# Kernel optimization log

Measured on AMD Instinct MI355X. Metric: run time of the kernel, lower is better.

## Reference

```python
import jax, jax.numpy as jnp
import numpy as np

N, E, T, B = 10000, 80000, 240000, 32
HF, EMB = 256, 64
EDGE_BINS, ANG_BINS = 80, 40
N_CONV = 12  # 4 alignn layers x 2 EGGC + 4 gcn EGGC


def layernorm(x, scale, bias):
    m = x.mean(-1, keepdims=True)
    v = ((x - m) ** 2).mean(-1, keepdims=True)
    return (x - m) / jnp.sqrt(v + 1e-5) * scale + bias


def mlp_layer(x, W, b, ln):
    # Linear -> LayerNorm -> SiLU
    return jax.nn.silu(layernorm(x @ W + b, ln[0], ln[1]))


def rbf(x, vmin, vmax, bins):
    centers = jnp.linspace(vmin, vmax, bins)
    gamma = 0.5 / ((vmax - vmin) / bins) ** 2
    return jnp.exp(-gamma * (x[..., None] - centers) ** 2)


def eggc(W, b, ln_s, ln_b, src, dst, h, e, n_nodes):
    """Edge-gated graph conv. W:[5,F,F] b:[5,F] order: src_gate,dst_gate,edge_gate,src_update,dst_update.
    ln_s/ln_b:[2,F] order: edges, nodes."""
    e_src = h @ W[0] + b[0]
    e_dst = h @ W[1] + b[1]
    sigma = jax.nn.sigmoid(e_src[src] + e_dst[dst] + e @ W[2] + b[2])  # [n_edges, F]
    e_out = layernorm(sigma * e, ln_s[0], ln_b[0])
    Bh = h @ W[4] + b[4]  # dst_update
    sum_sh = jax.ops.segment_sum(Bh[src] * sigma, dst, num_segments=n_nodes)
    sum_s = jax.ops.segment_sum(sigma, dst, num_segments=n_nodes)
    h_out = h @ W[3] + b[3] + sum_sh / (sum_s + 1e-8)  # src_update + gated mean
    return layernorm(h_out, ln_s[1], ln_b[1]), e_out


def setup_inputs() -> dict:
    key = jax.random.key(0)
    ks = jax.random.split(key, 24)
    rn = lambda k, shp: (jax.random.normal(k, shp, dtype=jnp.float32) * 0.05)
    ln_init = lambda f: jnp.stack([jnp.ones((f,), jnp.float32), jnp.zeros((f,), jnp.float32)])
    inp = {
        'atom_features': jax.random.normal(ks[0], (N, 92), dtype=jnp.float32),
        'bondlength': jax.random.uniform(ks[1], (E,), dtype=jnp.float32) * 8.0,
        'angle_h': jax.random.uniform(ks[2], (T,), dtype=jnp.float32) * 2.0 - 1.0,
        'src': jax.random.randint(ks[3], (E,), 0, N, dtype=jnp.int32),
        'dst': jax.random.randint(ks[4], (E,), 0, N, dtype=jnp.int32),
        'lg_src': jax.random.randint(ks[5], (T,), 0, E, dtype=jnp.int32),
        'lg_dst': jax.random.randint(ks[6], (T,), 0, E, dtype=jnp.int32),
        'graph_ids': jnp.sort(jax.random.randint(ks[7], (N,), 0, B)).astype(jnp.int32),
        'atom_W': rn(ks[8], (92, HF)), 'atom_b': jnp.zeros((HF,), jnp.float32), 'atom_ln': ln_init(HF),
        'edge_W1': rn(ks[9], (EDGE_BINS, EMB)), 'edge_b1': jnp.zeros((EMB,), jnp.float32), 'edge_ln1': ln_init(EMB),
        'edge_W2': rn(ks[10], (EMB, HF)), 'edge_b2': jnp.zeros((HF,), jnp.float32), 'edge_ln2': ln_init(HF),
        'ang_W1': rn(ks[11], (ANG_BINS, EMB)), 'ang_b1': jnp.zeros((EMB,), jnp.float32), 'ang_ln1': ln_init(EMB),
        'ang_W2': rn(ks[12], (EMB, HF)), 'ang_b2': jnp.zeros((HF,), jnp.float32), 'ang_ln2': ln_init(HF),
        'conv_W': rn(ks[13], (N_CONV, 5, HF, HF)),
        'conv_b': jnp.zeros((N_CONV, 5, HF), jnp.float32),
        'conv_ln_s': jnp.ones((N_CONV, 2, HF), jnp.float32),
        'conv_ln_b': jnp.zeros((N_CONV, 2, HF), jnp.float32),
    }
    return inp


def reference(atom_features, bondlength, angle_h, src, dst, lg_src, lg_dst, graph_ids,
              atom_W, atom_b, atom_ln, edge_W1, edge_b1, edge_ln1, edge_W2, edge_b2, edge_ln2,
              ang_W1, ang_b1, ang_ln1, ang_W2, ang_b2, ang_ln2,
              conv_W, conv_b, conv_ln_s, conv_ln_b):
    n_nodes = atom_features.shape[0]
    n_edges = bondlength.shape[0]
    # embeddings
    z = mlp_layer(mlp_layer(rbf(angle_h, -1.0, 1.0, ANG_BINS), ang_W1, ang_b1, ang_ln1), ang_W2, ang_b2, ang_ln2)
    x = mlp_layer(atom_features, atom_W, atom_b, atom_ln)
    y = mlp_layer(mlp_layer(rbf(bondlength, 0.0, 8.0, EDGE_BINS), edge_W1, edge_b1, edge_ln1), edge_W2, edge_b2, edge_ln2)
    # 4 ALIGNN layers: edge_update on line graph, then node_update on graph
    for i in range(4):
        j = 2 * i
        y, z = eggc(conv_W[j], conv_b[j], conv_ln_s[j], conv_ln_b[j], lg_src, lg_dst, y, z, n_edges)
        j = 2 * i + 1
        x, y = eggc(conv_W[j], conv_b[j], conv_ln_s[j], conv_ln_b[j], src, dst, x, y, n_nodes)
    # 4 GCN layers
    for i in range(4):
        j = 8 + i
        x, y = eggc(conv_W[j], conv_b[j], conv_ln_s[j], conv_ln_b[j], src, dst, x, y, n_nodes)
    # AvgPooling readout per graph
    sums = jax.ops.segment_sum(x, graph_ids, num_segments=B)
    counts = jax.ops.segment_sum(jnp.ones((n_nodes,), x.dtype), graph_ids, num_segments=B)
    return sums / jnp.maximum(counts, 1.0)[:, None]
```

## Files before the change

### kernel.cpp

```cpp
#include <hip/hip_runtime.h>
#include <hip/hip_bf16.h>

typedef unsigned short u16;
typedef unsigned int u32;
typedef __attribute__((ext_vector_type(8))) short short8;
typedef __attribute__((ext_vector_type(4))) float f32x4;

__device__ __forceinline__ float bf2f(u16 u) { return __uint_as_float(((u32)u) << 16); }
__device__ __forceinline__ u16 f2bf(float f) {
  u32 x = __float_as_uint(f);
  return (u16)((x + 0x7FFFu + ((x >> 16) & 1u)) >> 16);
}
__device__ __forceinline__ void up4(uint2 r, float* o) {
  o[0] = bf2f((u16)(r.x & 0xFFFF)); o[1] = bf2f((u16)(r.x >> 16));
  o[2] = bf2f((u16)(r.y & 0xFFFF)); o[3] = bf2f((u16)(r.y >> 16));
}
__device__ __forceinline__ uint2 pk4(const float* o) {
  uint2 r;
  r.x = (u32)f2bf(o[0]) | ((u32)f2bf(o[1]) << 16);
  r.y = (u32)f2bf(o[2]) | ((u32)f2bf(o[3]) << 16);
  return r;
}
__device__ __forceinline__ float wsum64(float v) {
#pragma unroll
  for (int o = 32; o > 0; o >>= 1) v += __shfl_xor(v, o, 64);
  return v;
}
__device__ __forceinline__ float sigm(float x) { return 1.0f / (1.0f + __expf(-x)); }

__global__ __launch_bounds__(256) void fill_kernel(float* __restrict__ out, int n, float v) {
  int i = blockIdx.x * 256 + threadIdx.x;
  if (i < n) out[i] = v;
}

__global__ __launch_bounds__(256) void wtrans(const float* __restrict__ in,
                                              u16* __restrict__ out, int R, int Ccols) {
  __shared__ float t[64][65];
  const float* ip = in + (size_t)blockIdx.z * R * Ccols;
  u16* op = out + (size_t)blockIdx.z * R * Ccols;
  int kb = blockIdx.x * 64, nb = blockIdx.y * 64;
  int lr = threadIdx.x >> 4, lc = (threadIdx.x & 15) * 4;
#pragma unroll
  for (int p = 0; p < 4; ++p) {
    int k = lr + p * 16;
    float4 v = *(const float4*)(ip + (size_t)(kb + k) * Ccols + nb + lc);
    t[k][lc + 0] = v.x; t[k][lc + 1] = v.y; t[k][lc + 2] = v.z; t[k][lc + 3] = v.w;
  }
  __syncthreads();
#pragma unroll
  for (int p = 0; p < 4; ++p) {
    int n = lr + p * 16;
    uint2 pk;
    pk.x = (u32)f2bf(t[lc + 0][n]) | ((u32)f2bf(t[lc + 1][n]) << 16);
    pk.y = (u32)f2bf(t[lc + 2][n]) | ((u32)f2bf(t[lc + 3][n]) << 16);
    *(uint2*)(op + (size_t)(nb + n) * R + kb + lc) = pk;
  }
}

__global__ __launch_bounds__(256) void csr_hist(const int* __restrict__ dst,
                                                int* __restrict__ hist, int ne) {
  int e = blockIdx.x * 256 + threadIdx.x;
  if (e < ne) atomicAdd(&hist[dst[e]], 1);
}
__global__ __launch_bounds__(1024) void scan1(const int* __restrict__ in,
                                              int* __restrict__ out1, int* __restrict__ bsum, int n) {
  __shared__ int s[1024];
  int i = blockIdx.x * 1024 + threadIdx.x;
  int v = (i < n) ? in[i] : 0;
  s[threadIdx.x] = v; __syncthreads();
  for (int off = 1; off < 1024; off <<= 1) {
    int t = (threadIdx.x >= (u32)off) ? s[threadIdx.x - off] : 0;
    __syncthreads();
    s[threadIdx.x] += t;
    __syncthreads();
  }
  if (i < n) out1[i] = s[threadIdx.x];
  if (threadIdx.x == 1023) bsum[blockIdx.x] = s[1023];
}
__global__ __launch_bounds__(128) void scan2(int* __restrict__ bsum, int nb) {
  __shared__ int s[128];
  int v = (threadIdx.x < (u32)nb) ? bsum[threadIdx.x] : 0;
  s[threadIdx.x] = v; __syncthreads();
  for (int off = 1; off < 128; off <<= 1) {
    int t = (threadIdx.x >= (u32)off) ? s[threadIdx.x - off] : 0;
    __syncthreads();
    s[threadIdx.x] += t;
    __syncthreads();
  }
  if (threadIdx.x < (u32)nb) bsum[threadIdx.x] = threadIdx.x ? s[threadIdx.x - 1] : 0;
}
__global__ __launch_bounds__(256) void scan3(int* __restrict__ offs,
                                             const int* __restrict__ bsum, int n) {
  int i = blockIdx.x * 256 + threadIdx.x;
  if (i == 0) offs[0] = 0;
  if (i < n) offs[1 + i] += bsum[i >> 10];
}
__global__ __launch_bounds__(256) void csr_scatter(const int* __restrict__ dst,
                                                   int* __restrict__ cursor,
                                                   const int* __restrict__ offs,
                                                   int* __restrict__ eid, int ne) {
  int e = blockIdx.x * 256 + threadIdx.x;
  if (e < ne) {
    int d = dst[e];
    int p = offs[d] + atomicAdd(&cursor[d], 1);
    eid[p] = e;
  }
}
__global__ __launch_bounds__(256) void inv_perm(const int* __restrict__ eid,
                                                int* __restrict__ pos, int n) {
  int i = blockIdx.x * 256 + threadIdx.x;
  if (i < n) pos[eid[i]] = i;
}
__global__ __launch_bounds__(256) void remap_k(const int* __restrict__ idx,
                                               const int* __restrict__ map,
                                               int* __restrict__ out, int n) {
  int i = blockIdx.x * 256 + threadIdx.x;
  if (i < n) out[i] = map[idx[i]];
}
__global__ __launch_bounds__(256) void compose_src(const int* __restrict__ eid,
                                                   const int* __restrict__ srcv,
                                                   const int* __restrict__ map,
                                                   int* __restrict__ out, int n) {
  int i = blockIdx.x * 256 + threadIdx.x;
  if (i < n) {
    int s = srcv[eid[i]];
    out[i] = map ? map[s] : s;
  }
}

__global__ __launch_bounds__(256) void embed_s1(
    const float* __restrict__ xin, const float* __restrict__ W1,
    const float* __restrict__ b1, const float* __restrict__ ln1,
    u16* __restrict__ t1, int rows, int bins, float vmin, float vmax,
    const int* __restrict__ perm) {
  int row = (blockIdx.x * 256 + threadIdx.x) >> 6;
  if (row >= rows) return;
  int lane = threadIdx.x & 63;
  float xv = xin[row];
  float rng = vmax - vmin;
  float step = rng / (float)(bins - 1);
  float gamma = 0.5f * ((float)bins / rng) * ((float)bins / rng);
  float rb = 0.f, rb2 = 0.f;
  if (lane < bins) {
    float d = xv - (vmin + lane * step);
    rb = __expf(-gamma * d * d);
  }
  if (bins > 64 && lane < bins - 64) {
    float d = xv - (vmin + (lane + 64) * step);
    rb2 = __expf(-gamma * d * d);
  }
  float u = b1[lane];
  int k1 = bins < 64 ? bins : 64;
  for (int k = 0; k < k1; ++k) {
    float rv = __shfl(rb, k, 64);
    u = fmaf(rv, W1[k * 64 + lane], u);
  }
  for (int k = 64; k < bins; ++k) {
    float rv = __shfl(rb2, k - 64, 64);
    u = fmaf(rv, W1[k * 64 + lane], u);
  }
  float s = wsum64(u), s2 = wsum64(u * u);
  float m = s * (1.f / 64.f), var = s2 * (1.f / 64.f) - m * m;
  float t = (u - m) * rsqrtf(var + 1e-5f) * ln1[lane] + ln1[64 + lane];
  int orow = perm ? perm[row] : row;
  t1[(size_t)orow * 64 + lane] = f2bf(t * sigm(t));
}

__global__ __launch_bounds__(256) void ln_silu(u16* __restrict__ buf,
                                               const float* __restrict__ ln, int rows) {
  int row = (blockIdx.x * 256 + threadIdx.x) >> 6;
  if (row >= rows) return;
  int lane = threadIdx.x & 63;
  int f = lane * 4;
  float v[4];
  up4(*(const uint2*)(buf + (size_t)row * 256 + f), v);
  float s = wsum64(v[0] + v[1] + v[2] + v[3]);
  float s2 = wsum64(v[0] * v[0] + v[1] * v[1] + v[2] * v[2] + v[3] * v[3]);
  float m = s * (1.f / 256.f);
  float rs = rsqrtf(s2 * (1.f / 256.f) - m * m + 1e-5f);
  float o[4];
#pragma unroll
  for (int k = 0; k < 4; ++k) {
    float t = (v[k] - m) * rs * ln[f + k] + ln[256 + f + k];
    o[k] = t * sigm(t);
  }
  *(uint2*)(buf + (size_t)row * 256 + f) = pk4(o);
}

__global__ __launch_bounds__(256) void atom_embed_kernel(
    const float* __restrict__ af, const float* __restrict__ W,
    const float* __restrict__ b, const float* __restrict__ ln,
    u16* __restrict__ out, int rows) {
  int row = blockIdx.x;
  if (row >= rows) return;
  __shared__ float a_s[92];
  __shared__ float red[8];
  int tid = threadIdx.x;
  if (tid < 92) a_s[tid] = af[(size_t)row * 92 + tid];
  __syncthreads();
  float v = b[tid];
#pragma unroll 4
  for (int k = 0; k < 92; ++k) v = fmaf(a_s[k], W[k * 256 + tid], v);
  float s = wsum64(v), s2 = wsum64(v * v);
  int lane = tid & 63, wid = tid >> 6;
  if (lane == 0) { red[wid] = s; red[4 + wid] = s2; }
  __syncthreads();
  s = red[0] + red[1] + red[2] + red[3];
  s2 = red[4] + red[5] + red[6] + red[7];
  float m = s * (1.f / 256.f), var = s2 * (1.f / 256.f) - m * m;
  float t = (v - m) * rsqrtf(var + 1e-5f) * ln[tid] + ln[256 + tid];
  out[(size_t)row * 256 + tid] = f2bf(t * sigm(t));
}

__global__ __launch_bounds__(256) void mfma_gemm(
    const u16* __restrict__ A, const u16* __restrict__ Wt,
    const float* __restrict__ bias, u16* __restrict__ C,
    int M, int K, int ldc, int slab_step) {
  int bm = blockIdx.x * 128;
  if (bm >= M) return;
  int bn = blockIdx.y * 128;
  int slab = (bn >> 8) * slab_step;
  const u16* Wp = Wt + (size_t)slab * 256 * K + (size_t)(bn & 255) * K;
  const float* bp = bias + slab * 256 + (bn & 255);
  int tid = threadIdx.x;
  int w = tid >> 6, lane = tid & 63;
  int q = lane >> 4, r = lane & 15;
  int m0 = (w & 1) * 64;
  int n0 = (w >> 1) * 64;
  const u16* aptr[4];
#pragma unroll
  for (int mi = 0; mi < 4; ++mi) {
    int m = bm + m0 + mi * 16 + r;
    m = m < M - 1 ? m : M - 1;
    aptr[mi] = A + (size_t)m * K + q * 8;
  }
  const u16* wptr[4];
#pragma unroll
  for (int ni = 0; ni < 4; ++ni)
    wptr[ni] = Wp + (size_t)(n0 + ni * 16 + r) * K + q * 8;
  f32x4 acc[4][4] = {};
  for (int kb = 0; kb < K; kb += 32) {
    short8 bfr[4], afr[4];
#pragma unroll
    for (int mi = 0; mi < 4; ++mi) bfr[mi] = *(const short8*)(aptr[mi] + kb);
#pragma unroll
    for (int ni = 0; ni < 4; ++ni) afr[ni] = *(const short8*)(wptr[ni] + kb);
#pragma unroll
    for (int mi = 0; mi < 4; ++mi)
#pragma unroll
      for (int ni = 0; ni < 4; ++ni)
        acc[mi][ni] = __builtin_amdgcn_mfma_f32_16x16x32_bf16(afr[ni], bfr[mi],
                                                              acc[mi][ni], 0, 0, 0);
  }
#pragma unroll
  for (int mi = 0; mi < 4; ++mi) {
    int m = bm + m0 + mi * 16 + r;
    if (m < M) {
#pragma unroll
      for (int ni = 0; ni < 4; ++ni) {
        int n = n0 + ni * 16 + q * 4;
        float4 bv = *(const float4*)(bp + n);
        uint2 o;
        o.x = (u32)f2bf(acc[mi][ni].x + bv.x) | ((u32)f2bf(acc[mi][ni].y + bv.y) << 16);
        o.y = (u32)f2bf(acc[mi][ni].z + bv.z) | ((u32)f2bf(acc[mi][ni].w + bv.w) << 16);
        *(uint2*)(C + (size_t)m * ldc + bn + n) = o;
      }
    }
  }
}

__global__ __launch_bounds__(512) void mega_eggc(
    u16* __restrict__ h, u16* __restrict__ e,
    const u16* __restrict__ G0Bh,
    const u16* __restrict__ Wt13, const float* __restrict__ b13,
    const u16* __restrict__ Wt2, const float* __restrict__ b2v,
    const int* __restrict__ src_perm, const int* __restrict__ offs,
    const float* __restrict__ lnS, const float* __restrict__ lnB, int nn) {
  __shared__ u16 g1ah[16][520];
  __shared__ u16 pe[64][264];
  int tid = threadIdx.x;
  int w = tid >> 6, lane = tid & 63;
  int q = lane >> 4, r = lane & 15;
  int v0 = blockIdx.x * 16;

  {
    int mrow = v0 + r; if (mrow > nn - 1) mrow = nn - 1;
    const u16* arow = h + (size_t)mrow * 256 + q * 8;
    f32x4 acc[4] = {};
    for (int kb = 0; kb < 256; kb += 32) {
      short8 af = *(const short8*)(arow + kb);
#pragma unroll
      for (int t = 0; t < 4; ++t) {
        int ng = (4 * w + t) * 16 + r;
        const u16* wrow = Wt13 + (size_t)(ng >> 8) * 2 * 65536 +
                          (size_t)(ng & 255) * 256 + q * 8;
        short8 wf = *(const short8*)(wrow + kb);
        acc[t] = __builtin_amdgcn_mfma_f32_16x16x32_bf16(wf, af, acc[t], 0, 0, 0);
      }
    }
#pragma unroll
    for (int t = 0; t < 4; ++t) {
      int nb = (4 * w + t) * 16 + q * 4;
      const float* bp = b13 + (nb >> 8) * 2 * 256 + (nb & 255);
      float o[4] = {acc[t].x + bp[0], acc[t].y + bp[1], acc[t].z + bp[2], acc[t].w + bp[3]};
      *(uint2*)&g1ah[r][nb] = pk4(o);
    }
  }
  __syncthreads();

  int f = lane * 4;
  int r0 = offs[v0];
  int vend = v0 + 16 < nn ? v0 + 16 : nn;
  int r1 = offs[vend];
  int vA = v0 + w * 2, vB = vA + 1;
  int eA0 = vA < nn ? offs[vA] : 0, eA1 = vA < nn ? offs[vA + 1] : 0;
  int eB0 = vB < nn ? offs[vB] : 0, eB1 = vB < nn ? offs[vB + 1] : 0;
  float sshA[4] = {0, 0, 0, 0}, ssmA[4] = {0, 0, 0, 0};
  float sshB[4] = {0, 0, 0, 0}, ssmB[4] = {0, 0, 0, 0};
  float lwe[4], lbe[4];
#pragma unroll
  for (int k = 0; k < 4; ++k) { lwe[k] = lnS[f + k]; lbe[k] = lnB[f + k]; }

  for (int ec = r0; ec < r1; ec += 64) {
    {
      const u16* w0p = Wt2 + (size_t)((2 * w) * 16 + r) * 256 + q * 8;
      const u16* w1p = Wt2 + (size_t)((2 * w + 1) * 16 + r) * 256 + q * 8;
      f32x4 acc[4][2] = {};
      for (int kb = 0; kb < 256; kb += 32) {
        short8 wf0 = *(const short8*)(w0p + kb);
        short8 wf1 = *(const short8*)(w1p + kb);
#pragma unroll
        for (int mt = 0; mt < 4; ++mt) {
          int erow = ec + mt * 16 + r;
          if (erow > r1 - 1) erow = r1 - 1;
          short8 af = *(const short8*)(e + (size_t)erow * 256 + kb + q * 8);
          acc[mt][0] = __builtin_amdgcn_mfma_f32_16x16x32_bf16(wf0, af, acc[mt][0], 0, 0, 0);
          acc[mt][1] = __builtin_amdgcn_mfma_f32_16x16x32_bf16(wf1, af, acc[mt][1], 0, 0, 0);
        }
      }
#pragma unroll
      for (int mt = 0; mt < 4; ++mt)
#pragma unroll
        for (int nt = 0; nt < 2; ++nt) {
          int nb = (2 * w + nt) * 16 + q * 4;
          float o[4] = {acc[mt][nt].x + b2v[nb], acc[mt][nt].y + b2v[nb + 1],
                        acc[mt][nt].z + b2v[nb + 2], acc[mt][nt].w + b2v[nb + 3]};
          *(uint2*)&pe[mt * 16 + r][nb] = pk4(o);
        }
    }
    __syncthreads();
    int ce = ec + 64 < r1 ? ec + 64 : r1;
#pragma unroll
    for (int jj = 0; jj < 2; ++jj) {
      int vv = jj ? vB : vA;
      int i0 = jj ? eB0 : eA0, i1 = jj ? eB1 : eA1;
      int lo = i0 > ec ? i0 : ec, hi = i1 < ce ? i1 : ce;
      for (int i = lo; i < hi; ++i) {
        int sv = src_perm[i];
        float g0[4], bh[4], pv[4], ev[4], g1v[4];
        up4(*(const uint2*)(G0Bh + (size_t)sv * 512 + f), g0);
        up4(*(const uint2*)(G0Bh + (size_t)sv * 512 + 256 + f), bh);
        up4(*(const uint2*)&pe[i - ec][f], pv);
        up4(*(const uint2*)(e + (size_t)i * 256 + f), ev);
        up4(*(const uint2*)&g1ah[vv - v0][f], g1v);
        float t[4];
        float ssum = 0.f, s2sum = 0.f;
#pragma unroll
        for (int k = 0; k < 4; ++k) {
          float sg = sigm(g0[k] + g1v[k] + pv[k]);
          t[k] = sg * ev[k];
          if (jj) { sshB[k] = fmaf(bh[k], sg, sshB[k]); ssmB[k] += sg; }
          else    { sshA[k] = fmaf(bh[k], sg, sshA[k]); ssmA[k] += sg; }
          ssum += t[k]; s2sum += t[k] * t[k];
        }
        float s1 = wsum64(ssum), s2 = wsum64(s2sum);
        float mn = s1 * (1.f / 256.f);
        float rs = rsqrtf(s2 * (1.f / 256.f) - mn * mn + 1e-5f);
        float o[4];
#pragma unroll
        for (int k = 0; k < 4; ++k) o[k] = (t[k] - mn) * rs * lwe[k] + lbe[k];
        *(uint2*)(e + (size_t)i * 256 + f) = pk4(o);
      }
    }
    __syncthreads();
  }
#pragma unroll
  for (int jj = 0; jj < 2; ++jj) {
    int vv = jj ? vB : vA;
    if (vv < nn) {
      float ah[4], tt[4];
      up4(*(const uint2*)&g1ah[vv - v0][256 + f], ah);
      float ssum = 0.f, s2sum = 0.f;
#pragma unroll
      for (int k = 0; k < 4; ++k) {
        float sh = jj ? sshB[k] : sshA[k];
        float sm = jj ? ssmB[k] : ssmA[k];
        tt[k] = ah[k] + sh / (sm + 1e-8f);
        ssum += tt[k]; s2sum += tt[k] * tt[k];
      }
      float s1 = wsum64(ssum), s2 = wsum64(s2sum);
      float mn = s1 * (1.f / 256.f);
      float rs = rsqrtf(s2 * (1.f / 256.f) - mn * mn + 1e-5f);
      float o[4];
#pragma unroll
      for (int k = 0; k < 4; ++k)
        o[k] = (tt[k] - mn) * rs * lnS[256 + f + k] + lnB[256 + f + k];
      *(uint2*)(h + (size_t)vv * 256 + f) = pk4(o);
    }
  }
}

__global__ __launch_bounds__(256) void pool_acc(
    const u16* __restrict__ x, const int* __restrict__ gid,
    float* __restrict__ out, float* __restrict__ cnt, int n) {
  int v = (blockIdx.x * 256 + threadIdx.x) >> 6;
  if (v >= n) return;
  int lane = threadIdx.x & 63;
  int f = lane * 4;
  int g = gid[v];
  float xv[4];
  up4(*(const uint2*)(x + (size_t)v * 256 + f), xv);
  float* p = out + (size_t)g * 256 + f;
  unsafeAtomicAdd(p + 0, xv[0]);
  unsafeAtomicAdd(p + 1, xv[1]);
  unsafeAtomicAdd(p + 2, xv[2]);
  unsafeAtomicAdd(p + 3, xv[3]);
  if (lane == 0) unsafeAtomicAdd(cnt + g, 1.0f);
}
__global__ __launch_bounds__(256) void pool_div(float* __restrict__ out,
                                                const float* __restrict__ cnt, int n) {
  int i = blockIdx.x * blockDim.x + threadIdx.x;
  if (i < n) out[i] /= fmaxf(cnt[i >> 8], 1.0f);
}

extern "C" void kernel_launch(void* const* d_in, const int* in_sizes, int n_in,
                              void* d_out, int out_size, void* d_ws, size_t ws_size,
                              hipStream_t stream) {
  const float* atom_features = (const float*)d_in[0];
  const float* bondlength    = (const float*)d_in[1];
  const float* angle_h       = (const float*)d_in[2];
  const int*   src           = (const int*)d_in[3];
  const int*   dst           = (const int*)d_in[4];
  const int*   lg_src        = (const int*)d_in[5];
  const int*   lg_dst        = (const int*)d_in[6];
  const int*   gid           = (const int*)d_in[7];
  const float* atom_W  = (const float*)d_in[8];
  const float* atom_b  = (const float*)d_in[9];
  const float* atom_ln = (const float*)d_in[10];
  const float* edge_W1 = (const float*)d_in[11];
  const float* edge_b1 = (const float*)d_in[12];
  const float* edge_ln1= (const float*)d_in[13];
  const float* edge_W2 = (const float*)d_in[14];
  const float* edge_b2 = (const float*)d_in[15];
  const float* edge_ln2= (const float*)d_in[16];
  const float* ang_W1  = (const float*)d_in[17];
  const float* ang_b1  = (const float*)d_in[18];
  const float* ang_ln1 = (const float*)d_in[19];
  const float* ang_W2  = (const float*)d_in[20];
  const float* ang_b2  = (const float*)d_in[21];
  const float* ang_ln2 = (const float*)d_in[22];
  const float* conv_W  = (const float*)d_in[23];
  const float* conv_b  = (const float*)d_in[24];
  const float* conv_lns= (const float*)d_in[25];
  const float* conv_lnb= (const float*)d_in[26];

  int N = in_sizes[0] / 92;
  int E = in_sizes[1];
  int T = in_sizes[2];

  char* ws = (char*)d_ws;
  size_t o = 0;
  auto alloc = [&](size_t bytes) { size_t r = o; o = (o + bytes + 255) & ~(size_t)255; return r; };
  u16* z     = (u16*)(ws + alloc((size_t)T * 512));
  u16* y     = (u16*)(ws + alloc((size_t)E * 512));
  u16* x     = (u16*)(ws + alloc((size_t)N * 512));
  int* offsL = (int*)(ws + alloc((size_t)(E + 1) * 4));
  int* offsA = (int*)(ws + alloc((size_t)(N + 1) * 4));
  int* spL   = (int*)(ws + alloc((size_t)T * 4));
  int* spA   = (int*)(ws + alloc((size_t)E * 4));
  int* pA    = (int*)(ws + alloc((size_t)E * 4));
  int* pL    = (int*)(ws + alloc((size_t)T * 4));
  int* eidL  = (int*)(ws + alloc((size_t)T * 4));
  int* eidA  = (int*)(ws + alloc((size_t)E * 4));
  int* ldSt  = (int*)(ws + alloc((size_t)T * 4));
  int* tmp   = (int*)(ws + alloc((size_t)(E > N ? E : N) * 4));
  int* bsum  = (int*)(ws + alloc(1024));
  float* cnt = (float*)(ws + alloc(1024));
  u16* WtAll = (u16*)(ws + alloc((size_t)12 * 5 * 65536 * 2));
  u16* WtAng = (u16*)(ws + alloc((size_t)16384 * 2));
  u16* WtEdg = (u16*)(ws + alloc((size_t)16384 * 2));
  size_t scratch_base = o;
  size_t need = scratch_base + (size_t)E * 1024;
  {
    size_t embed_need = scratch_base + ((size_t)T + E) * 128;
    if (embed_need > need) need = embed_need;
  }
  if (ws_size < need) {
    fill_kernel<<<(out_size + 255) / 256, 256, 0, stream>>>(
        (float*)d_out, out_size, (float)(ws_size >> 20));
    return;
  }

  wtrans<<<dim3(4, 4, 60), 256, 0, stream>>>(conv_W, WtAll, 256, 256);
  wtrans<<<dim3(1, 4, 1), 256, 0, stream>>>(ang_W2, WtAng, 64, 256);
  wtrans<<<dim3(1, 4, 1), 256, 0, stream>>>(edge_W2, WtEdg, 64, 256);

  auto build_csr = [&](const int* dvec, int ne_, int nn_, int* offs_, int* eid_) {
    hipMemsetAsync(tmp, 0, (size_t)nn_ * 4, stream);
    csr_hist<<<(ne_ + 255) / 256, 256, 0, stream>>>(dvec, tmp, ne_);
    int nb = (nn_ + 1023) / 1024;
    scan1<<<nb, 1024, 0, stream>>>(tmp, offs_ + 1, bsum, nn_);
    scan2<<<1, 128, 0, stream>>>(bsum, nb);
    scan3<<<(nn_ + 255) / 256, 256, 0, stream>>>(offs_, bsum, nn_);
    hipMemsetAsync(tmp, 0, (size_t)nn_ * 4, stream);
    csr_scatter<<<(ne_ + 255) / 256, 256, 0, stream>>>(dvec, tmp, offs_, eid_, ne_);
  };
  build_csr(dst, E, N, offsA, eidA);
  inv_perm<<<(E + 255) / 256, 256, 0, stream>>>(eidA, pA, E);
  compose_src<<<(E + 255) / 256, 256, 0, stream>>>(eidA, src, nullptr, spA, E);
  remap_k<<<(T + 255) / 256, 256, 0, stream>>>(lg_dst, pA, ldSt, T);
  build_csr(ldSt, T, E, offsL, eidL);
  inv_perm<<<(T + 255) / 256, 256, 0, stream>>>(eidL, pL, T);
  compose_src<<<(T + 255) / 256, 256, 0, stream>>>(eidL, lg_src, pA, spL, T);

  u16* t1T = (u16*)(ws + scratch_base);
  u16* t1E = t1T + (size_t)T * 64;
  embed_s1<<<(T + 3) / 4, 256, 0, stream>>>(angle_h, ang_W1, ang_b1, ang_ln1,
                                            t1T, T, 40, -1.f, 1.f, pL);
  embed_s1<<<(E + 3) / 4, 256, 0, stream>>>(bondlength, edge_W1, edge_b1, edge_ln1,
                                            t1E, E, 80, 0.f, 8.f, pA);
  mfma_gemm<<<dim3((T + 127) / 128, 2), 256, 0, stream>>>(
      t1T, WtAng, ang_b2, z, T, 64, 256, 1);
  mfma_gemm<<<dim3((E + 127) / 128, 2), 256, 0, stream>>>(
      t1E, WtEdg, edge_b2, y, E, 64, 256, 1);
  ln_silu<<<(T + 3) / 4, 256, 0, stream>>>(z, ang_ln2, T);
  ln_silu<<<(E + 3) / 4, 256, 0, stream>>>(y, edge_ln2, E);
  atom_embed_kernel<<<N, 256, 0, stream>>>(atom_features, atom_W, atom_b, atom_ln, x, N);

  u16* G0Bh = (u16*)(ws + scratch_base);
  for (int l = 0; l < 12; ++l) {
    const u16* WtL  = WtAll + (size_t)l * 5 * 65536;
    const float* bl = conv_b + (size_t)l * 5 * 256;
    const float* lnS = conv_lns + (size_t)l * 512;
    const float* lnB = conv_lnb + (size_t)l * 512;
    bool line = (l < 8) && ((l & 1) == 0);
    u16* h = line ? y : x;
    u16* e = line ? z : y;
    const int* sperm = line ? spL : spA;
    const int* offs  = line ? offsL : offsA;
    int nn = line ? E : N;

    mfma_gemm<<<dim3((nn + 127) / 128, 4), 256, 0, stream>>>(
        h, WtL, bl, G0Bh, nn, 256, 512, 4);
    mega_eggc<<<(nn + 15) / 16, 512, 0, stream>>>(
        h, e, G0Bh, WtL + 65536, bl + 256, WtL + 2 * 65536, bl + 2 * 256,
        sperm, offs, lnS, lnB, nn);
  }

  hipMemsetAsync(d_out, 0, (size_t)out_size * sizeof(float), stream);
  hipMemsetAsync(cnt, 0, 256 * sizeof(float), stream);
  pool_acc<<<(N + 3) / 4, 256, 0, stream>>>(x, gid, (float*)d_out, cnt, N);
  pool_div<<<(out_size + 255) / 256, 256, 0, stream>>>((float*)d_out, cnt, out_size);
}
```

Baseline: 5.469 ms.

## Shrink edge chunk to 32, raise occupancy, prefetch next edge gather

Cuts the per-chunk edge tile in the fused EGGC kernel from 64 to 32 rows. This halves the shared pe buffer and the MFMA accumulator registers, and adds a min-blocks launch bound hint to raise occupancy. The per-edge loop now software-prefetches the next edge's gathered G0/Bh and e rows, and hoists the per-node g1 load out of the loop, to hide gather latency. In exchange there are twice as many chunk iterations and syncthreads, and the Wt2 weight fragments are reloaded per chunk. Forcing occupancy may also cause register spills.

Result: slower. 6.757 ms (+23.6%).

```diff
diff --git a/kernel.cpp b/kernel.cpp
--- a/kernel.cpp
+++ b/kernel.cpp
@@ -269,7 +269,7 @@
   }
 }
 
-__global__ __launch_bounds__(512) void mega_eggc(
+__global__ __launch_bounds__(512, 6) void mega_eggc(
     u16* __restrict__ h, u16* __restrict__ e,
     const u16* __restrict__ G0Bh,
     const u16* __restrict__ Wt13, const float* __restrict__ b13,
@@ -277,7 +277,7 @@
     const int* __restrict__ src_perm, const int* __restrict__ offs,
     const float* __restrict__ lnS, const float* __restrict__ lnB, int nn) {
   __shared__ u16 g1ah[16][520];
-  __shared__ u16 pe[64][264];
+  __shared__ u16 pe[32][264];
   int tid = threadIdx.x;
   int w = tid >> 6, lane = tid & 63;
   int q = lane >> 4, r = lane & 15;
@@ -321,25 +321,27 @@
 #pragma unroll
   for (int k = 0; k < 4; ++k) { lwe[k] = lnS[f + k]; lbe[k] = lnB[f + k]; }
 
-  for (int ec = r0; ec < r1; ec += 64) {
+  for (int ec = r0; ec < r1; ec += 32) {
     {
       const u16* w0p = Wt2 + (size_t)((2 * w) * 16 + r) * 256 + q * 8;
       const u16* w1p = Wt2 + (size_t)((2 * w + 1) * 16 + r) * 256 + q * 8;
-      f32x4 acc[4][2] = {};
+      int er0 = ec + r;      if (er0 > r1 - 1) er0 = r1 - 1;
+      int er1 = ec + 16 + r; if (er1 > r1 - 1) er1 = r1 - 1;
+      const u16* ap0 = e + (size_t)er0 * 256 + q * 8;
+      const u16* ap1 = e + (size_t)er1 * 256 + q * 8;
+      f32x4 acc[2][2] = {};
       for (int kb = 0; kb < 256; kb += 32) {
         short8 wf0 = *(const short8*)(w0p + kb);
         short8 wf1 = *(const short8*)(w1p + kb);
-#pragma unroll
-        for (int mt = 0; mt < 4; ++mt) {
-          int erow = ec + mt * 16 + r;
-          if (erow > r1 - 1) erow = r1 - 1;
-          short8 af = *(const short8*)(e + (size_t)erow * 256 + kb + q * 8);
-          acc[mt][0] = __builtin_amdgcn_mfma_f32_16x16x32_bf16(wf0, af, acc[mt][0], 0, 0, 0);
-          acc[mt][1] = __builtin_amdgcn_mfma_f32_16x16x32_bf16(wf1, af, acc[mt][1], 0, 0, 0);
-        }
+        short8 af0 = *(const short8*)(ap0 + kb);
+        short8 af1 = *(const short8*)(ap1 + kb);
+        acc[0][0] = __builtin_amdgcn_mfma_f32_16x16x32_bf16(wf0, af0, acc[0][0], 0, 0, 0);
+        acc[0][1] = __builtin_amdgcn_mfma_f32_16x16x32_bf16(wf1, af0, acc[0][1], 0, 0, 0);
+        acc[1][0] = __builtin_amdgcn_mfma_f32_16x16x32_bf16(wf0, af1, acc[1][0], 0, 0, 0);
+        acc[1][1] = __builtin_amdgcn_mfma_f32_16x16x32_bf16(wf1, af1, acc[1][1], 0, 0, 0);
       }
 #pragma unroll
-      for (int mt = 0; mt < 4; ++mt)
+      for (int mt = 0; mt < 2; ++mt)
 #pragma unroll
         for (int nt = 0; nt < 2; ++nt) {
           int nb = (2 * w + nt) * 16 + q * 4;
@@ -349,20 +351,30 @@
         }
     }
     __syncthreads();
-    int ce = ec + 64 < r1 ? ec + 64 : r1;
+    int ce = ec + 32 < r1 ? ec + 32 : r1;
 #pragma unroll
     for (int jj = 0; jj < 2; ++jj) {
       int vv = jj ? vB : vA;
       int i0 = jj ? eB0 : eA0, i1 = jj ? eB1 : eA1;
       int lo = i0 > ec ? i0 : ec, hi = i1 < ce ? i1 : ce;
+      if (lo >= hi) continue;
+      float g1v[4];
+      up4(*(const uint2*)&g1ah[vv - v0][f], g1v);
+      int sv0 = src_perm[lo];
+      uint2 rg0 = *(const uint2*)(G0Bh + (size_t)sv0 * 512 + f);
+      uint2 rbh = *(const uint2*)(G0Bh + (size_t)sv0 * 512 + 256 + f);
+      uint2 rev = *(const uint2*)(e + (size_t)lo * 256 + f);
       for (int i = lo; i < hi; ++i) {
-        int sv = src_perm[i];
-        float g0[4], bh[4], pv[4], ev[4], g1v[4];
-        up4(*(const uint2*)(G0Bh + (size_t)sv * 512 + f), g0);
-        up4(*(const uint2*)(G0Bh + (size_t)sv * 512 + 256 + f), bh);
+        uint2 cg0 = rg0, cbh = rbh, cev = rev;
+        if (i + 1 < hi) {
+          int sv = src_perm[i + 1];
+          rg0 = *(const uint2*)(G0Bh + (size_t)sv * 512 + f);
+          rbh = *(const uint2*)(G0Bh + (size_t)sv * 512 + 256 + f);
+          rev = *(const uint2*)(e + (size_t)(i + 1) * 256 + f);
+        }
+        float g0[4], bh[4], pv[4], ev[4];
+        up4(cg0, g0); up4(cbh, bh); up4(cev, ev);
         up4(*(const uint2*)&pe[i - ec][f], pv);
-        up4(*(const uint2*)(e + (size_t)i * 256 + f), ev);
-        up4(*(const uint2*)&g1ah[vv - v0][f], g1v);
         float t[4];
         float ssum = 0.f, s2sum = 0.f;
 #pragma unroll
```

## Split EGGC into line/atom kernels with 16-lane-per-edge vectorized gather

Applied to the files above, without the earlier changes.

Reworks the edge-gating phase so each 16-lane group handles one destination node's edges with 16 features per lane. Two groups split the edges of a node and combine their partial sums with a shuffle. Gathers use 128-bit loads with one-step prefetch of the next source row, and the per-edge layernorm reduces across 16 lanes instead of 64. For the atom graph (small N), all four node projections are computed by one wider GEMM via a slab map instead of in-kernel MFMA, which removes redundant work from the mega kernel. The cost is higher register pressure and two code paths to maintain.

Measured after the change: 5.316 ms. -2.8%, faster.

```diff
diff --git a/kernel.cpp b/kernel.cpp
--- a/kernel.cpp
+++ b/kernel.cpp
@@ -21,9 +21,28 @@
   r.y = (u32)f2bf(o[2]) | ((u32)f2bf(o[3]) << 16);
   return r;
 }
+__device__ __forceinline__ void up8(uint4 r, float* o) {
+  o[0] = bf2f((u16)(r.x & 0xFFFF)); o[1] = bf2f((u16)(r.x >> 16));
+  o[2] = bf2f((u16)(r.y & 0xFFFF)); o[3] = bf2f((u16)(r.y >> 16));
+  o[4] = bf2f((u16)(r.z & 0xFFFF)); o[5] = bf2f((u16)(r.z >> 16));
+  o[6] = bf2f((u16)(r.w & 0xFFFF)); o[7] = bf2f((u16)(r.w >> 16));
+}
+__device__ __forceinline__ uint4 pk8(const float* o) {
+  uint4 r;
+  r.x = (u32)f2bf(o[0]) | ((u32)f2bf(o[1]) << 16);
+  r.y = (u32)f2bf(o[2]) | ((u32)f2bf(o[3]) << 16);
+  r.z = (u32)f2bf(o[4]) | ((u32)f2bf(o[5]) << 16);
+  r.w = (u32)f2bf(o[6]) | ((u32)f2bf(o[7]) << 16);
+  return r;
+}
 __device__ __forceinline__ float wsum64(float v) {
 #pragma unroll
   for (int o = 32; o > 0; o >>= 1) v += __shfl_xor(v, o, 64);
+  return v;
+}
+__device__ __forceinline__ float wsum16(float v) {
+#pragma unroll
+  for (int o = 8; o > 0; o >>= 1) v += __shfl_xor(v, o, 64);
   return v;
 }
 __device__ __forceinline__ float sigm(float x) { return 1.0f / (1.0f + __expf(-x)); }
@@ -215,11 +234,11 @@
 __global__ __launch_bounds__(256) void mfma_gemm(
     const u16* __restrict__ A, const u16* __restrict__ Wt,
     const float* __restrict__ bias, u16* __restrict__ C,
-    int M, int K, int ldc, int slab_step) {
+    int M, int K, int ldc, u32 smap) {
   int bm = blockIdx.x * 128;
   if (bm >= M) return;
   int bn = blockIdx.y * 128;
-  int slab = (bn >> 8) * slab_step;
+  int slab = (smap >> ((bn >> 8) * 8)) & 0xFF;
   const u16* Wp = Wt + (size_t)slab * 256 * K + (size_t)(bn & 255) * K;
   const float* bp = bias + slab * 256 + (bn & 255);
   int tid = threadIdx.x;
@@ -269,20 +288,20 @@
   }
 }
 
-__global__ __launch_bounds__(512) void mega_eggc(
-    u16* __restrict__ h, u16* __restrict__ e,
-    const u16* __restrict__ G0Bh,
+__global__ __launch_bounds__(512) void mega_line(
+    u16* __restrict__ h, u16* __restrict__ e, const u16* __restrict__ G0Bh,
     const u16* __restrict__ Wt13, const float* __restrict__ b13,
     const u16* __restrict__ Wt2, const float* __restrict__ b2v,
     const int* __restrict__ src_perm, const int* __restrict__ offs,
     const float* __restrict__ lnS, const float* __restrict__ lnB, int nn) {
   __shared__ u16 g1ah[16][520];
   __shared__ u16 pe[64][264];
+  __shared__ int oloc[17];
   int tid = threadIdx.x;
   int w = tid >> 6, lane = tid & 63;
   int q = lane >> 4, r = lane & 15;
   int v0 = blockIdx.x * 16;
-
+  if (tid < 17) { int v = v0 + tid; oloc[tid] = offs[v < nn ? v : nn]; }
   {
     int mrow = v0 + r; if (mrow > nn - 1) mrow = nn - 1;
     const u16* arow = h + (size_t)mrow * 256 + q * 8;
@@ -307,19 +326,20 @@
     }
   }
   __syncthreads();
-
-  int f = lane * 4;
-  int r0 = offs[v0];
-  int vend = v0 + 16 < nn ? v0 + 16 : nn;
-  int r1 = offs[vend];
-  int vA = v0 + w * 2, vB = vA + 1;
-  int eA0 = vA < nn ? offs[vA] : 0, eA1 = vA < nn ? offs[vA + 1] : 0;
-  int eB0 = vB < nn ? offs[vB] : 0, eB1 = vB < nn ? offs[vB + 1] : 0;
-  float sshA[4] = {0, 0, 0, 0}, ssmA[4] = {0, 0, 0, 0};
-  float sshB[4] = {0, 0, 0, 0}, ssmB[4] = {0, 0, 0, 0};
-  float lwe[4], lbe[4];
-#pragma unroll
-  for (int k = 0; k < 4; ++k) { lwe[k] = lnS[f + k]; lbe[k] = lnB[f + k]; }
+  int gl = lane & 15;
+  int qg = lane >> 4;
+  int dd = w * 2 + (qg >> 1);
+  int half = qg & 1;
+  int vv = v0 + dd;
+  int fb = gl * 16;
+  int r0 = oloc[0], r1 = oloc[16];
+  int d0 = oloc[dd], d1 = oloc[dd + 1];
+  float lwe[16], lbe[16];
+#pragma unroll
+  for (int k = 0; k < 16; ++k) { lwe[k] = lnS[fb + k]; lbe[k] = lnB[fb + k]; }
+  uint4 g1p0 = *(const uint4*)&g1ah[dd][fb];
+  uint4 g1p1 = *(const uint4*)&g1ah[dd][fb + 8];
+  float ssh[16] = {}, ssm[16] = {};
 
   for (int ec = r0; ec < r1; ec += 64) {
     {
@@ -349,64 +369,216 @@
         }
     }
     __syncthreads();
-    int ce = ec + 64 < r1 ? ec + 64 : r1;
-#pragma unroll
-    for (int jj = 0; jj < 2; ++jj) {
-      int vv = jj ? vB : vA;
-      int i0 = jj ? eB0 : eA0, i1 = jj ? eB1 : eA1;
-      int lo = i0 > ec ? i0 : ec, hi = i1 < ce ? i1 : ce;
-      for (int i = lo; i < hi; ++i) {
-        int sv = src_perm[i];
-        float g0[4], bh[4], pv[4], ev[4], g1v[4];
-        up4(*(const uint2*)(G0Bh + (size_t)sv * 512 + f), g0);
-        up4(*(const uint2*)(G0Bh + (size_t)sv * 512 + 256 + f), bh);
-        up4(*(const uint2*)&pe[i - ec][f], pv);
-        up4(*(const uint2*)(e + (size_t)i * 256 + f), ev);
-        up4(*(const uint2*)&g1ah[vv - v0][f], g1v);
-        float t[4];
-        float ssum = 0.f, s2sum = 0.f;
-#pragma unroll
-        for (int k = 0; k < 4; ++k) {
-          float sg = sigm(g0[k] + g1v[k] + pv[k]);
-          t[k] = sg * ev[k];
-          if (jj) { sshB[k] = fmaf(bh[k], sg, sshB[k]); ssmB[k] += sg; }
-          else    { sshA[k] = fmaf(bh[k], sg, sshA[k]); ssmA[k] += sg; }
-          ssum += t[k]; s2sum += t[k] * t[k];
+    {
+      int ce = ec + 64 < r1 ? ec + 64 : r1;
+      int i0 = d0 > ec ? d0 : ec;
+      int i1 = d1 < ce ? d1 : ce;
+      int is = i0 + half;
+      if (is < i1) {
+        int sv = src_perm[is];
+        uint4 pg0a = *(const uint4*)(G0Bh + (size_t)sv * 512 + fb);
+        uint4 pg0b = *(const uint4*)(G0Bh + (size_t)sv * 512 + fb + 8);
+        uint4 pbha = *(const uint4*)(G0Bh + (size_t)sv * 512 + 256 + fb);
+        uint4 pbhb = *(const uint4*)(G0Bh + (size_t)sv * 512 + 256 + fb + 8);
+        for (int i = is; i < i1; i += 2) {
+          uint4 cg0a = pg0a, cg0b = pg0b, cbha = pbha, cbhb = pbhb;
+          if (i + 2 < i1) {
+            int sv2 = src_perm[i + 2];
+            pg0a = *(const uint4*)(G0Bh + (size_t)sv2 * 512 + fb);
+            pg0b = *(const uint4*)(G0Bh + (size_t)sv2 * 512 + fb + 8);
+            pbha = *(const uint4*)(G0Bh + (size_t)sv2 * 512 + 256 + fb);
+            pbhb = *(const uint4*)(G0Bh + (size_t)sv2 * 512 + 256 + fb + 8);
+          }
+          float g0[16], bh[16], pv[16], ev[16], g1v[16];
+          up8(cg0a, g0); up8(cg0b, g0 + 8);
+          up8(cbha, bh); up8(cbhb, bh + 8);
+          up8(*(const uint4*)&pe[i - ec][fb], pv);
+          up8(*(const uint4*)&pe[i - ec][fb + 8], pv + 8);
+          up8(*(const uint4*)(e + (size_t)i * 256 + fb), ev);
+          up8(*(const uint4*)(e + (size_t)i * 256 + fb + 8), ev + 8);
+          up8(g1p0, g1v); up8(g1p1, g1v + 8);
+          float t[16];
+          float ssum = 0.f, s2sum = 0.f;
+#pragma unroll
+          for (int k = 0; k < 16; ++k) {
+            float sg = sigm(g0[k] + g1v[k] + pv[k]);
+            t[k] = sg * ev[k];
+            ssh[k] = fmaf(bh[k], sg, ssh[k]);
+            ssm[k] += sg;
+            ssum += t[k]; s2sum += t[k] * t[k];
+          }
+          float s1 = wsum16(ssum), s2 = wsum16(s2sum);
+          float mn = s1 * (1.f / 256.f);
+          float rs = rsqrtf(s2 * (1.f / 256.f) - mn * mn + 1e-5f);
+          float o[16];
+#pragma unroll
+          for (int k = 0; k < 16; ++k) o[k] = (t[k] - mn) * rs * lwe[k] + lbe[k];
+          *(uint4*)(e + (size_t)i * 256 + fb) = pk8(o);
+          *(uint4*)(e + (size_t)i * 256 + fb + 8) = pk8(o + 8);
         }
-        float s1 = wsum64(ssum), s2 = wsum64(s2sum);
-        float mn = s1 * (1.f / 256.f);
-        float rs = rsqrtf(s2 * (1.f / 256.f) - mn * mn + 1e-5f);
-        float o[4];
-#pragma unroll
-        for (int k = 0; k < 4; ++k) o[k] = (t[k] - mn) * rs * lwe[k] + lbe[k];
-        *(uint2*)(e + (size_t)i * 256 + f) = pk4(o);
       }
     }
     __syncthreads();
   }
 #pragma unroll
-  for (int jj = 0; jj < 2; ++jj) {
-    int vv = jj ? vB : vA;
-    if (vv < nn) {
-      float ah[4], tt[4];
-      up4(*(const uint2*)&g1ah[vv - v0][256 + f], ah);
-      float ssum = 0.f, s2sum = 0.f;
-#pragma unroll
-      for (int k = 0; k < 4; ++k) {
-        float sh = jj ? sshB[k] : sshA[k];
-        float sm = jj ? ssmB[k] : ssmA[k];
-        tt[k] = ah[k] + sh / (sm + 1e-8f);
-        ssum += tt[k]; s2sum += tt[k] * tt[k];
+  for (int k = 0; k < 16; ++k) {
+    ssh[k] += __shfl_xor(ssh[k], 16, 64);
+    ssm[k] += __shfl_xor(ssm[k], 16, 64);
+  }
+  if (half == 0 && vv < nn) {
+    float ah[16], tt[16];
+    up8(*(const uint4*)&g1ah[dd][256 + fb], ah);
+    up8(*(const uint4*)&g1ah[dd][256 + fb + 8], ah + 8);
+    float ssum = 0.f, s2sum = 0.f;
+#pragma unroll
+    for (int k = 0; k < 16; ++k) {
+      tt[k] = ah[k] + ssh[k] / (ssm[k] + 1e-8f);
+      ssum += tt[k]; s2sum += tt[k] * tt[k];
+    }
+    float s1 = wsum16(ssum), s2 = wsum16(s2sum);
+    float mn = s1 * (1.f / 256.f);
+    float rs = rsqrtf(s2 * (1.f / 256.f) - mn * mn + 1e-5f);
+    float o[16];
+#pragma unroll
+    for (int k = 0; k < 16; ++k)
+      o[k] = (tt[k] - mn) * rs * lnS[256 + fb + k] + lnB[256 + fb + k];
+    *(uint4*)(h + (size_t)vv * 256 + fb) = pk8(o);
+    *(uint4*)(h + (size_t)vv * 256 + fb + 8) = pk8(o + 8);
+  }
+}
+
+__global__ __launch_bounds__(512) void mega_atom(
+    u16* __restrict__ h, u16* __restrict__ e, const u16* __restrict__ GAll,
+    const u16* __restrict__ Wt2, const float* __restrict__ b2v,
+    const int* __restrict__ src_perm, const int* __restrict__ offs,
+    const float* __restrict__ lnS, const float* __restrict__ lnB, int nn) {
+  __shared__ u16 pe[64][264];
+  __shared__ int oloc[17];
+  int tid = threadIdx.x;
+  int w = tid >> 6, lane = tid & 63;
+  int q = lane >> 4, r = lane & 15;
+  int v0 = blockIdx.x * 16;
+  if (tid < 17) { int v = v0 + tid; oloc[tid] = offs[v < nn ? v : nn]; }
+  __syncthreads();
+  int gl = lane & 15;
+  int qg = lane >> 4;
+  int dd = w * 2 + (qg >> 1);
+  int half = qg & 1;
+  int vv = v0 + dd;
+  int fb = gl * 16;
+  int r0 = oloc[0], r1 = oloc[16];
+  int d0 = oloc[dd], d1 = oloc[dd + 1];
+  float lwe[16], lbe[16];
+#pragma unroll
+  for (int k = 0; k < 16; ++k) { lwe[k] = lnS[fb + k]; lbe[k] = lnB[fb + k]; }
+  int vc = vv < nn ? vv : nn - 1;
+  uint4 g1p0 = *(const uint4*)(GAll + (size_t)vc * 1024 + 256 + fb);
+  uint4 g1p1 = *(const uint4*)(GAll + (size_t)vc * 1024 + 256 + fb + 8);
+  float ssh[16] = {}, ssm[16] = {};
+
+  for (int ec = r0; ec < r1; ec += 64) {
+    {
+      const u16* w0p = Wt2 + (size_t)((2 * w) * 16 + r) * 256 + q * 8;
+      const u16* w1p = Wt2 + (size_t)((2 * w + 1) * 16 + r) * 256 + q * 8;
+      f32x4 acc[4][2] = {};
+      for (int kb = 0; kb < 256; kb += 32) {
+        short8 wf0 = *(const short8*)(w0p + kb);
+        short8 wf1 = *(const short8*)(w1p + kb);
+#pragma unroll
+        for (int mt = 0; mt < 4; ++mt) {
+          int erow = ec + mt * 16 + r;
+          if (erow > r1 - 1) erow = r1 - 1;
+          short8 af = *(const short8*)(e + (size_t)erow * 256 + kb + q * 8);
+          acc[mt][0] = __builtin_amdgcn_mfma_f32_16x16x32_bf16(wf0, af, acc[mt][0], 0, 0, 0);
+          acc[mt][1] = __builtin_amdgcn_mfma_f32_16x16x32_bf16(wf1, af, acc[mt][1], 0, 0, 0);
+        }
       }
-      float s1 = wsum64(ssum), s2 = wsum64(s2sum);
-      float mn = s1 * (1.f / 256.f);
-      float rs = rsqrtf(s2 * (1.f / 256.f) - mn * mn + 1e-5f);
-      float o[4];
-#pragma unroll
-      for (int k = 0; k < 4; ++k)
-        o[k] = (tt[k] - mn) * rs * lnS[256 + f + k] + lnB[256 + f + k];
-      *(uint2*)(h + (size_t)vv * 256 + f) = pk4(o);
-    }
+#pragma unroll
+      for (int mt = 0; mt < 4; ++mt)
+#pragma unroll
+        for (int nt = 0; nt < 2; ++nt) {
+          int nb = (2 * w + nt) * 16 + q * 4;
+          float o[4] = {acc[mt][nt].x + b2v[nb], acc[mt][nt].y + b2v[nb + 1],
+                        acc[mt][nt].z + b2v[nb + 2], acc[mt][nt].w + b2v[nb + 3]};
+          *(uint2*)&pe[mt * 16 + r][nb] = pk4(o);
+        }
+    }
+    __syncthreads();
+    {
+      int ce = ec + 64 < r1 ? ec + 64 : r1;
+      int i0 = d0 > ec ? d0 : ec;
+      int i1 = d1 < ce ? d1 : ce;
+      int is = i0 + half;
+      if (is < i1) {
+        int sv = src_perm[is];
+        uint4 pg0a = *(const uint4*)(GAll + (size_t)sv * 1024 + fb);
+        uint4 pg0b = *(const uint4*)(GAll + (size_t)sv * 1024 + fb + 8);
+        uint4 pbha = *(const uint4*)(GAll + (size_t)sv * 1024 + 768 + fb);
+        uint4 pbhb = *(const uint4*)(GAll + (size_t)sv * 1024 + 768 + fb + 8);
+        for (int i = is; i < i1; i += 2) {
+          uint4 cg0a = pg0a, cg0b = pg0b, cbha = pbha, cbhb = pbhb;
+          if (i + 2 < i1) {
+            int sv2 = src_perm[i + 2];
+            pg0a = *(const uint4*)(GAll + (size_t)sv2 * 1024 + fb);
+            pg0b = *(const uint4*)(GAll + (size_t)sv2 * 1024 + fb + 8);
+            pbha = *(const uint4*)(GAll + (size_t)sv2 * 1024 + 768 + fb);
+            pbhb = *(const uint4*)(GAll + (size_t)sv2 * 1024 + 768 + fb + 8);
+          }
+          float g0[16], bh[16], pv[16], ev[16], g1v[16];
+          up8(cg0a, g0); up8(cg0b, g0 + 8);
+          up8(cbha, bh); up8(cbhb, bh + 8);
+          up8(*(const uint4*)&pe[i - ec][fb], pv);
+          up8(*(const uint4*)&pe[i - ec][fb + 8], pv + 8);
+          up8(*(const uint4*)(e + (size_t)i * 256 + fb), ev);
+          up8(*(const uint4*)(e + (size_t)i * 256 + fb + 8), ev + 8);
+          up8(g1p0, g1v); up8(g1p1, g1v + 8);
+          float t[16];
+          float ssum = 0.f, s2sum = 0.f;
+#pragma unroll
+          for (int k = 0; k < 16; ++k) {
+            float sg = sigm(g0[k] + g1v[k] + pv[k]);
+            t[k] = sg * ev[k];
+            ssh[k] = fmaf(bh[k], sg, ssh[k]);
+            ssm[k] += sg;
+            ssum += t[k]; s2sum += t[k] * t[k];
+          }
+          float s1 = wsum16(ssum), s2 = wsum16(s2sum);
+          float mn = s1 * (1.f / 256.f);
+          float rs = rsqrtf(s2 * (1.f / 256.f) - mn * mn + 1e-5f);
+          float o[16];
+#pragma unroll
+          for (int k = 0; k < 16; ++k) o[k] = (t[k] - mn) * rs * lwe[k] + lbe[k];
+          *(uint4*)(e + (size_t)i * 256 + fb) = pk8(o);
+          *(uint4*)(e + (size_t)i * 256 + fb + 8) = pk8(o + 8);
+        }
+      }
+    }
+    __syncthreads();
+  }
+#pragma unroll
+  for (int k = 0; k < 16; ++k) {
+    ssh[k] += __shfl_xor(ssh[k], 16, 64);
+    ssm[k] += __shfl_xor(ssm[k], 16, 64);
+  }
+  if (half == 0 && vv < nn) {
+    float ah[16], tt[16];
+    up8(*(const uint4*)(GAll + (size_t)vv * 1024 + 512 + fb), ah);
+    up8(*(const uint4*)(GAll + (size_t)vv * 1024 + 512 + fb + 8), ah + 8);
+    float ssum = 0.f, s2sum = 0.f;
+#pragma unroll
+    for (int k = 0; k < 16; ++k) {
+      tt[k] = ah[k] + ssh[k] / (ssm[k] + 1e-8f);
+      ssum += tt[k]; s2sum += tt[k] * tt[k];
+    }
+    float s1 = wsum16(ssum), s2 = wsum16(s2sum);
+    float mn = s1 * (1.f / 256.f);
+    float rs = rsqrtf(s2 * (1.f / 256.f) - mn * mn + 1e-5f);
+    float o[16];
+#pragma unroll
+    for (int k = 0; k < 16; ++k)
+      o[k] = (tt[k] - mn) * rs * lnS[256 + fb + k] + lnB[256 + fb + k];
+    *(uint4*)(h + (size_t)vv * 256 + fb) = pk8(o);
+    *(uint4*)(h + (size_t)vv * 256 + fb + 8) = pk8(o + 8);
   }
 }
 
@@ -530,31 +702,34 @@
   embed_s1<<<(E + 3) / 4, 256, 0, stream>>>(bondlength, edge_W1, edge_b1, edge_ln1,
                                             t1E, E, 80, 0.f, 8.f, pA);
   mfma_gemm<<<dim3((T + 127) / 128, 2), 256, 0, stream>>>(
-      t1T, WtAng, ang_b2, z, T, 64, 256, 1);
+      t1T, WtAng, ang_b2, z, T, 64, 256, 0u);
   mfma_gemm<<<dim3((E + 127) / 128, 2), 256, 0, stream>>>(
-      t1E, WtEdg, edge_b2, y, E, 64, 256, 1);
+      t1E, WtEdg, edge_b2, y, E, 64, 256, 0u);
   ln_silu<<<(T + 3) / 4, 256, 0, stream>>>(z, ang_ln2, T);
   ln_silu<<<(E + 3) / 4, 256, 0, stream>>>(y, edge_ln2, E);
   atom_embed_kernel<<<N, 256, 0, stream>>>(atom_features, atom_W, atom_b, atom_ln, x, N);
 
-  u16* G0Bh = (u16*)(ws + scratch_base);
   for (int l = 0; l < 12; ++l) {
     const u16* WtL  = WtAll + (size_t)l * 5 * 65536;
     const float* bl = conv_b + (size_t)l * 5 * 256;
     const float* lnS = conv_lns + (size_t)l * 512;
     const float* lnB = conv_lnb + (size_t)l * 512;
     bool line = (l < 8) && ((l & 1) == 0);
-    u16* h = line ? y : x;
-    u16* e = line ? z : y;
-    const int* sperm = line ? spL : spA;
-    const int* offs  = line ? offsL : offsA;
-    int nn = line ? E : N;
-
-    mfma_gemm<<<dim3((nn + 127) / 128, 4), 256, 0, stream>>>(
-        h, WtL, bl, G0Bh, nn, 256, 512, 4);
-    mega_eggc<<<(nn + 15) / 16, 512, 0, stream>>>(
-        h, e, G0Bh, WtL + 65536, bl + 256, WtL + 2 * 65536, bl + 2 * 256,
-        sperm, offs, lnS, lnB, nn);
+    if (line) {
+      u16* G0Bh = (u16*)(ws + scratch_base);
+      mfma_gemm<<<dim3((E + 127) / 128, 4), 256, 0, stream>>>(
+          y, WtL, bl, G0Bh, E, 256, 512, 0u | (4u << 8));
+      mega_line<<<(E + 15) / 16, 512, 0, stream>>>(
+          y, z, G0Bh, WtL + 65536, bl + 256, WtL + 2 * 65536, bl + 2 * 256,
+          spL, offsL, lnS, lnB, E);
+    } else {
+      u16* GAll = (u16*)(ws + scratch_base);
+      mfma_gemm<<<dim3((N + 127) / 128, 8), 256, 0, stream>>>(
+          x, WtL, bl, GAll, N, 256, 1024, 0u | (1u << 8) | (3u << 16) | (4u << 24));
+      mega_atom<<<(N + 15) / 16, 512, 0, stream>>>(
+          x, y, GAll, WtL + 2 * 65536, bl + 2 * 256,
+          spA, offsA, lnS, lnB, N);
+    }
   }
 
   hipMemsetAsync(d_out, 0, (size_t)out_size * sizeof(float), stream);
```
